# Kernel optimization log

Hardware: AMD Instinct MI355X
Metric: run time of the kernel (lower is better)

## Reference

```python
import jax, jax.numpy as jnp
import numpy as np

CARRY_DIM = 384
READ_DIM = 128
D_MODEL = CARRY_DIM + READ_DIM  # 512
VOCAB = 128
NUM_FF = 7
B, T = 128, 1024


def _pm1(key, shape):
    # random +/-1 floats, matching random_pm1 in the torch source
    return jnp.where(jax.random.bernoulli(key, 0.5, shape), 1.0, -1.0).astype(jnp.float32)


def setup_inputs() -> dict:
    key = jax.random.key(0)
    k0, k1, k2, k3, k4 = jax.random.split(key, 5)
    return {
        "tokens": jax.random.randint(k0, (B, T), 0, VOCAB, dtype=jnp.int32),
        "initial": _pm1(k1, (D_MODEL,)),
        "embed": _pm1(k2, (VOCAB, READ_DIM)),
        "ff": _pm1(k3, (NUM_FF, D_MODEL, D_MODEL)),
        "ff_thresh": jnp.zeros((NUM_FF, D_MODEL), jnp.float32),
        "head": _pm1(k4, (READ_DIM, VOCAB)),
    }


def reference(tokens, initial, embed, ff, ff_thresh, head):
    # tokens:[B,T] int32; all params are +/-1 floats (the unpacked view of the
    # bit-packed int32 buffers; popcount GEMM == +/-1 matmul in integer arithmetic).
    b = tokens.shape[0]
    emb = jnp.swapaxes(embed[tokens], 0, 1)          # [T,B,READ_DIM]
    state0 = jnp.broadcast_to(initial, (b, D_MODEL))  # [B,512] +/-1

    def step(state, e):
        # replace read slice with current token embedding
        x = jnp.concatenate([state[:, :CARRY_DIM], e], axis=1)  # [B,512]

        def layer(xc, wt):
            w, t = wt  # w:[512,512], t:[512]
            # binary matmul (popcount dot in +/-1 space) + threshold nonlinearity
            return jnp.where(xc @ w >= t, 1.0, -1.0).astype(jnp.float32), None

        x, _ = jax.lax.scan(layer, x, (ff, ff_thresh))
        logits = x[:, CARRY_DIM:] @ head  # [B,VOCAB] integer-valued counts
        return x, logits

    _, logits = jax.lax.scan(step, state0, emb)  # logits:[T,B,V]
    return jnp.swapaxes(logits, 0, 1)            # [B,T,V]
```

## Files before the change

kernel.cpp:

```cpp
#include <hip/hip_runtime.h>
#include <hip/hip_bf16.h>
#include <stdint.h>

#define NUM_FF 7
#define DM 512
#define CARRY 384
#define RD 128
#define VOCABN 128
#define BATCH 128
#define TLEN 1024

__global__ void pack_ff_kernel(const float* __restrict__ ff, uint32_t* __restrict__ ffp) {
    int idx = blockIdx.x * blockDim.x + threadIdx.x;
    if (idx >= NUM_FF * 16 * DM) return;
    int j = idx & (DM - 1);
    int k = (idx >> 9) & 15;
    int l = idx >> 13;
    const float* base = ff + (size_t)l * DM * DM + (size_t)(k * 32) * DM + j;
    uint32_t w = 0;
#pragma unroll
    for (int i = 0; i < 32; ++i)
        w |= (base[(size_t)i * DM] > 0.0f ? 1u : 0u) << i;
    ffp[idx] = w;
}

__global__ void pack_small_kernel(const float* __restrict__ embed,
                                  const float* __restrict__ head,
                                  const float* __restrict__ initial,
                                  uint32_t* __restrict__ embp,
                                  uint32_t* __restrict__ headp,
                                  uint32_t* __restrict__ initp) {
    int idx = threadIdx.x;
    {
        int v = idx >> 2, k = idx & 3;
        uint32_t w = 0;
#pragma unroll
        for (int i = 0; i < 32; ++i)
            w |= (embed[v * RD + k * 32 + i] > 0.0f ? 1u : 0u) << i;
        embp[idx] = w;
    }
    {
        int k = idx >> 7, v = idx & 127;
        uint32_t w = 0;
#pragma unroll
        for (int i = 0; i < 32; ++i)
            w |= (head[(k * 32 + i) * VOCABN + v] > 0.0f ? 1u : 0u) << i;
        headp[idx] = w;
    }
    if (idx < 16) {
        uint32_t w = 0;
#pragma unroll
        for (int i = 0; i < 32; ++i)
            w |= (initial[idx * 32 + i] > 0.0f ? 1u : 0u) << i;
        initp[idx] = w;
    }
}

__device__ __forceinline__ int bdot16(uint4 s0, uint4 s1, uint4 s2, uint4 s3,
                                      const uint32_t* __restrict__ w) {
    int a = __popc(s0.x ^ w[0]);
    a += __popc(s0.y ^ w[1]);
    a += __popc(s0.z ^ w[2]);
    a += __popc(s0.w ^ w[3]);
    a += __popc(s1.x ^ w[4]);
    a += __popc(s1.y ^ w[5]);
    a += __popc(s1.z ^ w[6]);
    a += __popc(s1.w ^ w[7]);
    int b = __popc(s2.x ^ w[8]);
    b += __popc(s2.y ^ w[9]);
    b += __popc(s2.z ^ w[10]);
    b += __popc(s2.w ^ w[11]);
    b += __popc(s3.x ^ w[12]);
    b += __popc(s3.y ^ w[13]);
    b += __popc(s3.z ^ w[14]);
    b += __popc(s3.w ^ w[15]);
    return a + b;
}

#define SYNCB asm volatile("s_waitcnt lgkmcnt(0)\n\ts_barrier" ::: "memory")

__launch_bounds__(256, 1)
__global__ void brnn_kernel(const int* __restrict__ tokens,
                            const float* __restrict__ ff_thresh,
                            const uint32_t* __restrict__ ffp,
                            const uint32_t* __restrict__ embp,
                            const uint32_t* __restrict__ headp,
                            const uint32_t* __restrict__ initp,
                            float* __restrict__ out) {
    const int b = blockIdx.x;
    const int tid = threadIdx.x;
    const int wv = tid >> 6;
    const int lane = tid & 63;
    const int c0 = (wv << 7) | lane;
    const int c1 = c0 + 64;

    __shared__ uint4 xq0[4], xq1[4];
    __shared__ uint4 hxv;
    __shared__ uint32_t emb_lds[VOCABN * 4];
    __shared__ int tok_lds[TLEN + 4];

    uint32_t wA[NUM_FF][16], wB[NUM_FF][16];
#pragma unroll
    for (int l = 0; l < NUM_FF; ++l)
#pragma unroll
        for (int k = 0; k < 16; ++k) {
            wA[l][k] = ffp[l * (16 * DM) + k * DM + c0];
            wB[l][k] = ffp[l * (16 * DM) + k * DM + c1];
        }
    float thA[NUM_FF], thB[NUM_FF];
#pragma unroll
    for (int l = 0; l < NUM_FF; ++l) {
        thA[l] = ff_thresh[l * DM + c0];
        thB[l] = ff_thresh[l * DM + c1];
    }
    uint32_t h0 = 0, h1 = 0, h2 = 0, h3 = 0;
    if (tid < VOCABN) {
        h0 = headp[0 * VOCABN + tid];
        h1 = headp[1 * VOCABN + tid];
        h2 = headp[2 * VOCABN + tid];
        h3 = headp[3 * VOCABN + tid];
    }
    emb_lds[tid] = embp[tid];
    emb_lds[tid + 256] = embp[tid + 256];
    tok_lds[tid] = tokens[b * TLEN + tid];
    tok_lds[tid + 256] = tokens[b * TLEN + tid + 256];
    tok_lds[tid + 512] = tokens[b * TLEN + tid + 512];
    tok_lds[tid + 768] = tokens[b * TLEN + tid + 768];
    if (tid == 0) tok_lds[TLEN] = 0;
    if (tid < 16) ((uint32_t*)xq0)[tid] = initp[tid];
    __syncthreads();
    if (tid < 4) ((uint32_t*)xq0)[12 + tid] = emb_lds[tok_lds[0] * 4 + tid];
    __syncthreads();

    float* outb = out + (size_t)b * TLEN * VOCABN;

#define LAYER(l, SRCQ, DSTQ) do {                                              \
        uint4 s0 = (SRCQ)[0], s1 = (SRCQ)[1], s2 = (SRCQ)[2], s3 = (SRCQ)[3]; \
        int accA = bdot16(s0, s1, s2, s3, wA[l]);                              \
        int accB = bdot16(s0, s1, s2, s3, wB[l]);                              \
        unsigned long long m0 = __ballot((float)(DM - 2 * accA) >= thA[l]);    \
        unsigned long long m1 = __ballot((float)(DM - 2 * accB) >= thB[l]);    \
        if (lane == 0)                                                         \
            (DSTQ)[wv] = make_uint4((uint32_t)m0, (uint32_t)(m0 >> 32),        \
                                    (uint32_t)m1, (uint32_t)(m1 >> 32));       \
        SYNCB;                                                                 \
    } while (0)

#define LAYERF(l, SRCQ, DSTQ, tnext) do {                                      \
        uint4 s0 = (SRCQ)[0], s1 = (SRCQ)[1], s2 = (SRCQ)[2], s3 = (SRCQ)[3]; \
        int accA = bdot16(s0, s1, s2, s3, wA[l]);                              \
        int accB = bdot16(s0, s1, s2, s3, wB[l]);                              \
        unsigned long long m0 = __ballot((float)(DM - 2 * accA) >= thA[l]);    \
        unsigned long long m1 = __ballot((float)(DM - 2 * accB) >= thB[l]);    \
        if (lane == 0) {                                                       \
            uint4 v = make_uint4((uint32_t)m0, (uint32_t)(m0 >> 32),           \
                                 (uint32_t)m1, (uint32_t)(m1 >> 32));          \
            if (wv < 3) (DSTQ)[wv] = v;                                        \
            else hxv = v;                                                      \
        }                                                                      \
        if (tid < 4)                                                           \
            ((uint32_t*)(DSTQ))[12 + tid] = emb_lds[tok_lds[tnext] * 4 + tid]; \
        SYNCB;                                                                 \
    } while (0)

#define HEADOUT(t) do {                                                        \
        if (tid < VOCABN) {                                                    \
            uint4 hv = hxv;                                                    \
            int hc = __popc(hv.x ^ h0) + __popc(hv.y ^ h1) +                   \
                     __popc(hv.z ^ h2) + __popc(hv.w ^ h3);                    \
            outb[(t) * VOCABN + tid] = (float)(RD - 2 * hc);                   \
        }                                                                      \
    } while (0)

    for (int t = 0; t < TLEN; t += 2) {
        LAYER(0, xq0, xq1);
        LAYER(1, xq1, xq0);
        LAYER(2, xq0, xq1);
        LAYER(3, xq1, xq0);
        LAYER(4, xq0, xq1);
        LAYER(5, xq1, xq0);
        LAYERF(6, xq0, xq1, t + 1);
        HEADOUT(t);
        LAYER(0, xq1, xq0);
        LAYER(1, xq0, xq1);
        LAYER(2, xq1, xq0);
        LAYER(3, xq0, xq1);
        LAYER(4, xq1, xq0);
        LAYER(5, xq0, xq1);
        LAYERF(6, xq1, xq0, t + 2);
        HEADOUT(t + 1);
    }
#undef LAYER
#undef LAYERF
#undef HEADOUT
}

extern "C" void kernel_launch(void* const* d_in, const int* in_sizes, int n_in,
                              void* d_out, int out_size, void* d_ws, size_t ws_size,
                              hipStream_t stream) {
    const int* tokens = (const int*)d_in[0];
    const float* initial = (const float*)d_in[1];
    const float* embed = (const float*)d_in[2];
    const float* ff = (const float*)d_in[3];
    const float* ff_thresh = (const float*)d_in[4];
    const float* head = (const float*)d_in[5];
    float* out = (float*)d_out;

    uint32_t* ffp = (uint32_t*)d_ws;
    uint32_t* embp = ffp + NUM_FF * 16 * DM;
    uint32_t* headp = embp + 512;
    uint32_t* initp = headp + 512;

    pack_ff_kernel<<<(NUM_FF * 16 * DM + 255) / 256, 256, 0, stream>>>(ff, ffp);
    pack_small_kernel<<<1, 512, 0, stream>>>(embed, head, initial, embp, headp, initp);
    brnn_kernel<<<BATCH, 256, 0, stream>>>(tokens, ff_thresh, ffp, embp, headp, initp, out);
}
```

Measured before the change: 2.198 ms.

## Use 512 threads per block with one output column each and integer thresholds

Doubles the block to 512 threads, so each thread computes a single output column per layer instead of two. This halves the serial popcount chain per thread between barriers. Float thresholds are precomputed into integer popcount cutoffs by a new pack kernel, which removes the float convert and compare. The head computation is spread across all eight waves, and the next token's embedding word is fetched early so its lookup leaves the barrier-critical path. In exchange, each barrier now synchronises eight waves instead of four.

```diff
diff --git a/kernel.cpp b/kernel.cpp
--- a/kernel.cpp
+++ b/kernel.cpp
@@ -1,14 +1,16 @@
 #include <hip/hip_runtime.h>
 #include <hip/hip_bf16.h>
 #include <stdint.h>
+#include <math.h>
 
 #define NUM_FF 7
 #define DM 512
-#define CARRY 384
 #define RD 128
 #define VOCABN 128
 #define BATCH 128
 #define TLEN 1024
+
+typedef unsigned int u32x16 __attribute__((ext_vector_type(16)));
 
 __global__ void pack_ff_kernel(const float* __restrict__ ff, uint32_t* __restrict__ ffp) {
     int idx = blockIdx.x * blockDim.x + threadIdx.x;
@@ -22,6 +24,12 @@
     for (int i = 0; i < 32; ++i)
         w |= (base[(size_t)i * DM] > 0.0f ? 1u : 0u) << i;
     ffp[idx] = w;
+}
+
+__global__ void pack_thresh_kernel(const float* __restrict__ th, int* __restrict__ it) {
+    int idx = blockIdx.x * blockDim.x + threadIdx.x;
+    if (idx < NUM_FF * DM)
+        it[idx] = (int)floor((512.0 - (double)th[idx]) * 0.5);
 }
 
 __global__ void pack_small_kernel(const float* __restrict__ embed,
@@ -56,8 +64,7 @@
     }
 }
 
-__device__ __forceinline__ int bdot16(uint4 s0, uint4 s1, uint4 s2, uint4 s3,
-                                      const uint32_t* __restrict__ w) {
+__device__ __forceinline__ int bdot(uint4 s0, uint4 s1, uint4 s2, uint4 s3, u32x16 w) {
     int a = __popc(s0.x ^ w[0]);
     a += __popc(s0.y ^ w[1]);
     a += __popc(s0.z ^ w[2]);
@@ -66,23 +73,23 @@
     a += __popc(s1.y ^ w[5]);
     a += __popc(s1.z ^ w[6]);
     a += __popc(s1.w ^ w[7]);
-    int b = __popc(s2.x ^ w[8]);
-    b += __popc(s2.y ^ w[9]);
-    b += __popc(s2.z ^ w[10]);
-    b += __popc(s2.w ^ w[11]);
-    b += __popc(s3.x ^ w[12]);
-    b += __popc(s3.y ^ w[13]);
-    b += __popc(s3.z ^ w[14]);
-    b += __popc(s3.w ^ w[15]);
-    return a + b;
+    int c = __popc(s2.x ^ w[8]);
+    c += __popc(s2.y ^ w[9]);
+    c += __popc(s2.z ^ w[10]);
+    c += __popc(s2.w ^ w[11]);
+    c += __popc(s3.x ^ w[12]);
+    c += __popc(s3.y ^ w[13]);
+    c += __popc(s3.z ^ w[14]);
+    c += __popc(s3.w ^ w[15]);
+    return a + c;
 }
 
 #define SYNCB asm volatile("s_waitcnt lgkmcnt(0)\n\ts_barrier" ::: "memory")
 
-__launch_bounds__(256, 1)
+__launch_bounds__(512, 2)
 __global__ void brnn_kernel(const int* __restrict__ tokens,
-                            const float* __restrict__ ff_thresh,
                             const uint32_t* __restrict__ ffp,
+                            const int* __restrict__ ithr,
                             const uint32_t* __restrict__ embp,
                             const uint32_t* __restrict__ headp,
                             const uint32_t* __restrict__ initp,
@@ -91,42 +98,37 @@
     const int tid = threadIdx.x;
     const int wv = tid >> 6;
     const int lane = tid & 63;
-    const int c0 = (wv << 7) | lane;
-    const int c1 = c0 + 64;
 
     __shared__ uint4 xq0[4], xq1[4];
-    __shared__ uint4 hxv;
-    __shared__ uint32_t emb_lds[VOCABN * 4];
-    __shared__ int tok_lds[TLEN + 4];
-
-    uint32_t wA[NUM_FF][16], wB[NUM_FF][16];
-#pragma unroll
-    for (int l = 0; l < NUM_FF; ++l)
-#pragma unroll
-        for (int k = 0; k < 16; ++k) {
-            wA[l][k] = ffp[l * (16 * DM) + k * DM + c0];
-            wB[l][k] = ffp[l * (16 * DM) + k * DM + c1];
-        }
-    float thA[NUM_FF], thB[NUM_FF];
-#pragma unroll
-    for (int l = 0; l < NUM_FF; ++l) {
-        thA[l] = ff_thresh[l * DM + c0];
-        thB[l] = ff_thresh[l * DM + c1];
-    }
-    uint32_t h0 = 0, h1 = 0, h2 = 0, h3 = 0;
-    if (tid < VOCABN) {
-        h0 = headp[0 * VOCABN + tid];
-        h1 = headp[1 * VOCABN + tid];
-        h2 = headp[2 * VOCABN + tid];
-        h3 = headp[3 * VOCABN + tid];
-    }
+    __shared__ uint4 hx4;
+    __shared__ uint32_t emb_lds[DM];
+    __shared__ int tok_lds[TLEN + 2];
+
+    u32x16 W0, W1, W2, W3, W4, W5, W6;
+#define LOADW(L) { u32x16 w_;                                                  \
+        _Pragma("unroll")                                                      \
+        for (int k = 0; k < 16; ++k) w_[k] = ffp[(L) * (16 * DM) + k * DM + tid]; \
+        W##L = w_; }
+    LOADW(0) LOADW(1) LOADW(2) LOADW(3) LOADW(4) LOADW(5) LOADW(6)
+#undef LOADW
+    const int it0 = ithr[0 * DM + tid];
+    const int it1 = ithr[1 * DM + tid];
+    const int it2 = ithr[2 * DM + tid];
+    const int it3 = ithr[3 * DM + tid];
+    const int it4 = ithr[4 * DM + tid];
+    const int it5 = ithr[5 * DM + tid];
+    const int it6 = ithr[6 * DM + tid];
+
+    const int hvv = (wv << 4) | (lane & 15);
+    const uint32_t h0 = headp[0 * VOCABN + hvv];
+    const uint32_t h1 = headp[1 * VOCABN + hvv];
+    const uint32_t h2 = headp[2 * VOCABN + hvv];
+    const uint32_t h3 = headp[3 * VOCABN + hvv];
+
     emb_lds[tid] = embp[tid];
-    emb_lds[tid + 256] = embp[tid + 256];
     tok_lds[tid] = tokens[b * TLEN + tid];
-    tok_lds[tid + 256] = tokens[b * TLEN + tid + 256];
     tok_lds[tid + 512] = tokens[b * TLEN + tid + 512];
-    tok_lds[tid + 768] = tokens[b * TLEN + tid + 768];
-    if (tid == 0) tok_lds[TLEN] = 0;
+    if (tid == 0) { tok_lds[TLEN] = 0; tok_lds[TLEN + 1] = 0; }
     if (tid < 16) ((uint32_t*)xq0)[tid] = initp[tid];
     __syncthreads();
     if (tid < 4) ((uint32_t*)xq0)[12 + tid] = emb_lds[tok_lds[0] * 4 + tid];
@@ -134,65 +136,56 @@
 
     float* outb = out + (size_t)b * TLEN * VOCABN;
 
-#define LAYER(l, SRCQ, DSTQ) do {                                              \
-        uint4 s0 = (SRCQ)[0], s1 = (SRCQ)[1], s2 = (SRCQ)[2], s3 = (SRCQ)[3]; \
-        int accA = bdot16(s0, s1, s2, s3, wA[l]);                              \
-        int accB = bdot16(s0, s1, s2, s3, wB[l]);                              \
-        unsigned long long m0 = __ballot((float)(DM - 2 * accA) >= thA[l]);    \
-        unsigned long long m1 = __ballot((float)(DM - 2 * accB) >= thB[l]);    \
+#define LAYER(L, SRCQ, DSTQ) do {                                              \
+        const uint4* xb_ = (const uint4*)(SRCQ);                               \
+        uint4 s0 = xb_[0], s1 = xb_[1], s2 = xb_[2], s3 = xb_[3];              \
+        int acc = bdot(s0, s1, s2, s3, W##L);                                  \
+        unsigned long long m = __ballot(acc <= it##L);                         \
         if (lane == 0)                                                         \
-            (DSTQ)[wv] = make_uint4((uint32_t)m0, (uint32_t)(m0 >> 32),        \
-                                    (uint32_t)m1, (uint32_t)(m1 >> 32));       \
+            ((uint2*)(DSTQ))[wv] = make_uint2((uint32_t)m, (uint32_t)(m >> 32)); \
         SYNCB;                                                                 \
     } while (0)
 
-#define LAYERF(l, SRCQ, DSTQ, tnext) do {                                      \
-        uint4 s0 = (SRCQ)[0], s1 = (SRCQ)[1], s2 = (SRCQ)[2], s3 = (SRCQ)[3]; \
-        int accA = bdot16(s0, s1, s2, s3, wA[l]);                              \
-        int accB = bdot16(s0, s1, s2, s3, wB[l]);                              \
-        unsigned long long m0 = __ballot((float)(DM - 2 * accA) >= thA[l]);    \
-        unsigned long long m1 = __ballot((float)(DM - 2 * accB) >= thB[l]);    \
+#define LAYERF(SRCQ, DSTQ) do {                                                \
+        const uint4* xb_ = (const uint4*)(SRCQ);                               \
+        uint4 s0 = xb_[0], s1 = xb_[1], s2 = xb_[2], s3 = xb_[3];              \
+        int acc = bdot(s0, s1, s2, s3, W6);                                    \
+        unsigned long long m = __ballot(acc <= it6);                           \
         if (lane == 0) {                                                       \
-            uint4 v = make_uint4((uint32_t)m0, (uint32_t)(m0 >> 32),           \
-                                 (uint32_t)m1, (uint32_t)(m1 >> 32));          \
-            if (wv < 3) (DSTQ)[wv] = v;                                        \
-            else hxv = v;                                                      \
+            uint2 v_ = make_uint2((uint32_t)m, (uint32_t)(m >> 32));           \
+            if (wv < 6) ((uint2*)(DSTQ))[wv] = v_;                             \
+            else ((uint2*)&hx4)[wv - 6] = v_;                                  \
         }                                                                      \
-        if (tid < 4)                                                           \
-            ((uint32_t*)(DSTQ))[12 + tid] = emb_lds[tok_lds[tnext] * 4 + tid]; \
+        if (wv == 7 && lane < 4) ((uint32_t*)(DSTQ))[12 + lane] = embw;        \
         SYNCB;                                                                 \
     } while (0)
 
-#define HEADOUT(t) do {                                                        \
-        if (tid < VOCABN) {                                                    \
-            uint4 hv = hxv;                                                    \
-            int hc = __popc(hv.x ^ h0) + __popc(hv.y ^ h1) +                   \
-                     __popc(hv.z ^ h2) + __popc(hv.w ^ h3);                    \
-            outb[(t) * VOCABN + tid] = (float)(RD - 2 * hc);                   \
+#define STEP(AQ, BQ, T) do {                                                   \
+                      \
+        uint32_t embw = 0;                                                     \
+        if (wv == 7) embw = emb_lds[tok_lds[(T) + 1] * 4 + (lane & 3)];        \
+        LAYER(0, AQ, BQ);                                                      \
+        LAYER(1, BQ, AQ);                                                      \
+        LAYER(2, AQ, BQ);                                                      \
+        LAYER(3, BQ, AQ);                                                      \
+        LAYER(4, AQ, BQ);                                                      \
+        LAYER(5, BQ, AQ);                                                      \
+        LAYERF(AQ, BQ);                                                        \
+        uint4 hv_ = hx4;                                                       \
+        if (lane < 16) {                                                       \
+            int hc = __popc(hv_.x ^ h0) + __popc(hv_.y ^ h1) +                 \
+                     __popc(hv_.z ^ h2) + __popc(hv_.w ^ h3);                  \
+            outb[(T) * VOCABN + hvv] = (float)(RD - 2 * hc);                   \
         }                                                                      \
     } while (0)
 
     for (int t = 0; t < TLEN; t += 2) {
-        LAYER(0, xq0, xq1);
-        LAYER(1, xq1, xq0);
-        LAYER(2, xq0, xq1);
-        LAYER(3, xq1, xq0);
-        LAYER(4, xq0, xq1);
-        LAYER(5, xq1, xq0);
-        LAYERF(6, xq0, xq1, t + 1);
-        HEADOUT(t);
-        LAYER(0, xq1, xq0);
-        LAYER(1, xq0, xq1);
-        LAYER(2, xq1, xq0);
-        LAYER(3, xq0, xq1);
-        LAYER(4, xq1, xq0);
-        LAYER(5, xq0, xq1);
-        LAYERF(6, xq1, xq0, t + 2);
-        HEADOUT(t + 1);
+        STEP(xq0, xq1, t);
+        STEP(xq1, xq0, t + 1);
     }
 #undef LAYER
 #undef LAYERF
-#undef HEADOUT
+#undef STEP
 }
 
 extern "C" void kernel_launch(void* const* d_in, const int* in_sizes, int n_in,
@@ -210,8 +203,10 @@
     uint32_t* embp = ffp + NUM_FF * 16 * DM;
     uint32_t* headp = embp + 512;
     uint32_t* initp = headp + 512;
+    int* ithr = (int*)(initp + 16);
 
     pack_ff_kernel<<<(NUM_FF * 16 * DM + 255) / 256, 256, 0, stream>>>(ff, ffp);
+    pack_thresh_kernel<<<(NUM_FF * DM + 255) / 256, 256, 0, stream>>>(ff_thresh, ithr);
     pack_small_kernel<<<1, 512, 0, stream>>>(embed, head, initial, embp, headp, initp);
-    brnn_kernel<<<BATCH, 256, 0, stream>>>(tokens, ff_thresh, ffp, embp, headp, initp, out);
-}
+    brnn_kernel<<<BATCH, 512, 0, stream>>>(tokens, ffp, ithr, embp, headp, initp, out);
+}
```

New measurement: 1.951 ms. 11.3% less time.
